# Performance work log

Measured on AMD Instinct MI355X. Metric: run time of the kernel, lower is better.

Reference implementation:

```python
import jax, jax.numpy as jnp
import numpy as np

B, T, DIM = 4, 1024, 512
H, DH, NK, K = 8, 128, 256, 16
LN_EPS = 1e-5


def setup_inputs() -> dict:
    key = jax.random.key(0)
    ks = jax.random.split(key, 5)
    std_q = 1.0 / np.sqrt(DIM)
    std_k = 1.0 / np.sqrt(DH)
    std_v = 1.0 / np.sqrt(DIM)
    x = jax.random.normal(ks[0], (B, T, DIM), dtype=jnp.float32)
    Wq = jax.random.normal(ks[1], (2 * H * DH, DIM), dtype=jnp.float32) * std_q
    ln_g = jnp.ones((DH,), dtype=jnp.float32)
    ln_b = jnp.zeros((DH,), dtype=jnp.float32)
    keys = jax.random.normal(ks[2], (H, NK, 2, DH), dtype=jnp.float32) * std_k
    values = jax.random.normal(ks[3], (NK * NK, DIM), dtype=jnp.float32) * std_v
    return {"x": x, "Wq": Wq, "ln_g": ln_g, "ln_b": ln_b, "keys": keys, "values": values}


def _layernorm(q, g, b):
    mu = q.mean(-1, keepdims=True)
    var = ((q - mu) ** 2).mean(-1, keepdims=True)
    return (q - mu) * jax.lax.rsqrt(var + LN_EPS) * g + b


def reference(x, Wq, ln_g, ln_b, keys, values):
    b, t, _ = x.shape
    # queries: [b, t, 2*h*dh] -> [b, t, p=2, h, dh]
    q = jnp.einsum('btd,qd->btq', x, Wq).reshape(b, t, 2, H, DH)
    q = _layernorm(q, ln_g, ln_b)
    # product-key dots: [b, t, h, p, n]
    dots = jnp.einsum('btphd,hnpd->bthpn', q, keys)
    scores, idx = jax.lax.top_k(dots, K)          # [b,t,h,2,K]
    sx, sy = scores[..., 0, :], scores[..., 1, :]
    ix, iy = idx[..., 0, :], idx[..., 1, :]
    # cross product of the two halves -> K*K candidates
    all_scores = (sx[..., :, None] + sy[..., None, :]).reshape(b, t, H, K * K)
    all_idx = (ix[..., :, None] * NK + iy[..., None, :]).reshape(b, t, H, K * K)
    final_scores, final_pos = jax.lax.top_k(all_scores, K)      # [b,t,h,K]
    value_idx = jnp.take_along_axis(all_idx, final_pos, axis=-1)
    attn = jax.nn.softmax(final_scores, axis=-1)
    value_idx = value_idx.reshape(b * t, H * K)
    attn = attn.reshape(b * t, H * K)
    # EmbeddingBag(sum) with per-sample weights
    gathered = values[value_idx]                  # [(b t), h*K, dim]
    out = jnp.einsum('nk,nkd->nd', attn, gathered)
    return out.reshape(b, t, DIM)
```

## Files before the change

### kernel.cpp

```cpp
#include <hip/hip_runtime.h>
#include <hip/hip_bf16.h>
#include <math.h>
#include <stdint.h>

#define BT   4096
#define QD   2048
#define DIMK 512
#define NH   8
#define DHD  128
#define NKEY 256
#define TK   16

__global__ __launch_bounds__(256) void qproj_ln(
    const float* __restrict__ x, const float* __restrict__ Wq,
    const float* __restrict__ lng, const float* __restrict__ lnb,
    float* __restrict__ q) {
  __shared__ float As[8][128];
  __shared__ float Bs[8][128];
  const int br = blockIdx.x;
  const int bc = blockIdx.y;
  const int tid = threadIdx.x;
  const int ty = tid >> 4, tx = tid & 15;
  const int lr = tid >> 1, lc = (tid & 1) * 4;

  const float* xA = x  + (size_t)(br * 128 + lr) * DIMK + lc;
  const float* wB = Wq + (size_t)(bc * 128 + lr) * DIMK + lc;

  float acc[8][8];
  #pragma unroll
  for (int i = 0; i < 8; i++)
    #pragma unroll
    for (int j = 0; j < 8; j++) acc[i][j] = 0.f;

  for (int kt = 0; kt < DIMK; kt += 8) {
    float4 a4 = *(const float4*)(xA + kt);
    float4 b4 = *(const float4*)(wB + kt);
    __syncthreads();
    As[lc + 0][lr] = a4.x; As[lc + 1][lr] = a4.y;
    As[lc + 2][lr] = a4.z; As[lc + 3][lr] = a4.w;
    Bs[lc + 0][lr] = b4.x; Bs[lc + 1][lr] = b4.y;
    Bs[lc + 2][lr] = b4.z; Bs[lc + 3][lr] = b4.w;
    __syncthreads();
    #pragma unroll
    for (int kk = 0; kk < 8; kk++) {
      float a[8], b[8];
      #pragma unroll
      for (int i = 0; i < 8; i++) a[i] = As[kk][ty * 8 + i];
      #pragma unroll
      for (int j = 0; j < 8; j++) b[j] = Bs[kk][tx * 8 + j];
      #pragma unroll
      for (int i = 0; i < 8; i++)
        #pragma unroll
        for (int j = 0; j < 8; j++)
          acc[i][j] = fmaf(a[i], b[j], acc[i][j]);
    }
  }

  float g[8], bb[8];
  #pragma unroll
  for (int j = 0; j < 8; j++) { g[j] = lng[tx * 8 + j]; bb[j] = lnb[tx * 8 + j]; }

  #pragma unroll
  for (int i = 0; i < 8; i++) {
    float s = 0.f;
    #pragma unroll
    for (int j = 0; j < 8; j++) s += acc[i][j];
    #pragma unroll
    for (int m = 1; m < 16; m <<= 1) s += __shfl_xor(s, m);
    const float mu = s * (1.f / 128.f);
    float s2 = 0.f;
    #pragma unroll
    for (int j = 0; j < 8; j++) { float d = acc[i][j] - mu; s2 = fmaf(d, d, s2); }
    #pragma unroll
    for (int m = 1; m < 16; m <<= 1) s2 += __shfl_xor(s2, m);
    const float rstd = rsqrtf(s2 * (1.f / 128.f) + 1e-5f);
    float o[8];
    #pragma unroll
    for (int j = 0; j < 8; j++)
      o[j] = (acc[i][j] - mu) * rstd * g[j] + bb[j];
    float* qp = q + (size_t)(br * 128 + ty * 8 + i) * QD + bc * 128 + tx * 8;
    *(float4*)(qp)     = make_float4(o[0], o[1], o[2], o[3]);
    *(float4*)(qp + 4) = make_float4(o[4], o[5], o[6], o[7]);
  }
}

__global__ __launch_bounds__(256) void dots_gemm(
    const float* __restrict__ q, const float* __restrict__ keys,
    float* __restrict__ S) {
  __shared__ float As[8][128];
  __shared__ float Bs[8][128];
  const int br = blockIdx.x;
  const int bc = blockIdx.y;
  const int hp = blockIdx.z;
  const int h = hp >> 1, p = hp & 1;
  const int tid = threadIdx.x;
  const int ty = tid >> 4, tx = tid & 15;
  const int lr = tid >> 1, lc = (tid & 1) * 4;

  const float* qA = q + (size_t)(br * 128 + lr) * QD + p * 1024 + h * 128 + lc;
  const float* kB = keys + ((size_t)((h * 256 + bc * 128 + lr) * 2 + p)) * 128 + lc;

  float acc[8][8];
  #pragma unroll
  for (int i = 0; i < 8; i++)
    #pragma unroll
    for (int j = 0; j < 8; j++) acc[i][j] = 0.f;

  for (int kt = 0; kt < DHD; kt += 8) {
    float4 a4 = *(const float4*)(qA + kt);
    float4 b4 = *(const float4*)(kB + kt);
    __syncthreads();
    As[lc + 0][lr] = a4.x; As[lc + 1][lr] = a4.y;
    As[lc + 2][lr] = a4.z; As[lc + 3][lr] = a4.w;
    Bs[lc + 0][lr] = b4.x; Bs[lc + 1][lr] = b4.y;
    Bs[lc + 2][lr] = b4.z; Bs[lc + 3][lr] = b4.w;
    __syncthreads();
    #pragma unroll
    for (int kk = 0; kk < 8; kk++) {
      float a[8], b[8];
      #pragma unroll
      for (int i = 0; i < 8; i++) a[i] = As[kk][ty * 8 + i];
      #pragma unroll
      for (int j = 0; j < 8; j++) b[j] = Bs[kk][tx * 8 + j];
      #pragma unroll
      for (int i = 0; i < 8; i++)
        #pragma unroll
        for (int j = 0; j < 8; j++)
          acc[i][j] = fmaf(a[i], b[j], acc[i][j]);
    }
  }

  float* Sp = S + (size_t)hp * BT * NKEY;
  #pragma unroll
  for (int i = 0; i < 8; i++) {
    float* pp = Sp + (size_t)(br * 128 + ty * 8 + i) * NKEY + bc * 128 + tx * 8;
    *(float4*)(pp)     = make_float4(acc[i][0], acc[i][1], acc[i][2], acc[i][3]);
    *(float4*)(pp + 4) = make_float4(acc[i][4], acc[i][5], acc[i][6], acc[i][7]);
  }
}

__device__ __forceinline__ uint32_t f2u(float f) {
  uint32_t b = __float_as_uint(f);
  return b ^ ((uint32_t)((int32_t)b >> 31) | 0x80000000u);
}
__device__ __forceinline__ float u2f(uint32_t u) {
  uint32_t b = (u & 0x80000000u) ? (u ^ 0x80000000u) : ~u;
  return __uint_as_float(b);
}
__device__ __forceinline__ int cnt_lt(uint64_t m) {
  return __builtin_amdgcn_mbcnt_hi((uint32_t)(m >> 32),
         __builtin_amdgcn_mbcnt_lo((uint32_t)m, 0));
}

__global__ __launch_bounds__(64) void topk_combine(
    const float* __restrict__ S, float* __restrict__ W, int* __restrict__ I) {
  const int bt = blockIdx.x;
  const int h  = blockIdx.y;
  const int l  = threadIdx.x;

  __shared__ __align__(16) float sx_lds[16], sy_lds[16], w_lds[16];
  __shared__ __align__(16) int   ix_lds[16], iy_lds[16], vi_lds[16];

  const float* S0 = S + ((size_t)(h * 2 + 0) * BT + bt) * NKEY;
  const float* S1 = S + ((size_t)(h * 2 + 1) * BT + bt) * NKEY;
  float4 v0 = *(const float4*)(S0 + l * 4);
  float4 v1 = *(const float4*)(S1 + l * 4);
  float s0[4] = {v0.x, v0.y, v0.z, v0.w};
  float s1[4] = {v1.x, v1.y, v1.z, v1.w};
  uint32_t u0[4], u1[4];
  #pragma unroll
  for (int r = 0; r < 4; r++) { u0[r] = f2u(s0[r]); u1[r] = f2u(s1[r]); }

  uint32_t pfx0 = 0u, pfx1 = 0u;
  #pragma unroll
  for (int b = 31; b >= 0; b--) {
    const uint32_t t0 = pfx0 | (1u << b);
    const uint32_t t1 = pfx1 | (1u << b);
    int c0 = 0, c1 = 0;
    #pragma unroll
    for (int r = 0; r < 4; r++) {
      c0 += __popcll(__ballot(u0[r] >= t0));
      c1 += __popcll(__ballot(u1[r] >= t1));
    }
    if (c0 >= TK) pfx0 = t0;
    if (c1 >= TK) pfx1 = t1;
  }

  {
    uint64_t mgt[4], meq[4];
    int ngt = 0, below_gt = 0, below_eq = 0;
    #pragma unroll
    for (int r = 0; r < 4; r++) {
      mgt[r] = __ballot(u0[r] > pfx0);
      meq[r] = __ballot(u0[r] == pfx0);
      ngt += __popcll(mgt[r]);
      below_gt += cnt_lt(mgt[r]);
      below_eq += cnt_lt(meq[r]);
    }
    const int need = TK - ngt;
    int loc_gt = 0, loc_eq = 0;
    #pragma unroll
    for (int r = 0; r < 4; r++) {
      const bool isgt = (u0[r] > pfx0), iseq = (u0[r] == pfx0);
      int slot = -1;
      if (isgt) slot = below_gt + loc_gt;
      else if (iseq) { const int re = below_eq + loc_eq; if (re < need) slot = ngt + re; }
      if (slot >= 0) { sx_lds[slot] = s0[r]; ix_lds[slot] = l * 4 + r; }
      loc_gt += isgt; loc_eq += iseq;
    }
  }
  {
    uint64_t mgt[4], meq[4];
    int ngt = 0, below_gt = 0, below_eq = 0;
    #pragma unroll
    for (int r = 0; r < 4; r++) {
      mgt[r] = __ballot(u1[r] > pfx1);
      meq[r] = __ballot(u1[r] == pfx1);
      ngt += __popcll(mgt[r]);
      below_gt += cnt_lt(mgt[r]);
      below_eq += cnt_lt(meq[r]);
    }
    const int need = TK - ngt;
    int loc_gt = 0, loc_eq = 0;
    #pragma unroll
    for (int r = 0; r < 4; r++) {
      const bool isgt = (u1[r] > pfx1), iseq = (u1[r] == pfx1);
      int slot = -1;
      if (isgt) slot = below_gt + loc_gt;
      else if (iseq) { const int re = below_eq + loc_eq; if (re < need) slot = ngt + re; }
      if (slot >= 0) { sy_lds[slot] = s1[r]; iy_lds[slot] = l * 4 + r; }
      loc_gt += isgt; loc_eq += iseq;
    }
  }
  __syncthreads();

  const float sxv = sx_lds[l >> 2];
  const float4 syv = *(const float4*)&sy_lds[(l & 3) * 4];
  float cv[4] = {sxv + syv.x, sxv + syv.y, sxv + syv.z, sxv + syv.w};
  uint32_t uc[4];
  #pragma unroll
  for (int r = 0; r < 4; r++) uc[r] = f2u(cv[r]);

  uint32_t pfx2 = 0u;
  #pragma unroll
  for (int b = 31; b >= 0; b--) {
    const uint32_t t2 = pfx2 | (1u << b);
    int c2 = 0;
    #pragma unroll
    for (int r = 0; r < 4; r++) c2 += __popcll(__ballot(uc[r] >= t2));
    if (c2 >= TK) pfx2 = t2;
  }

  const float tau2f = u2f(pfx2);
  const int ivx = ix_lds[l >> 2];
  const int4 iyv = *(const int4*)&iy_lds[(l & 3) * 4];
  const int iy4[4] = {iyv.x, iyv.y, iyv.z, iyv.w};
  {
    uint64_t mgt[4], meq[4];
    int ngt = 0, below_gt = 0, below_eq = 0;
    #pragma unroll
    for (int r = 0; r < 4; r++) {
      mgt[r] = __ballot(uc[r] > pfx2);
      meq[r] = __ballot(uc[r] == pfx2);
      ngt += __popcll(mgt[r]);
      below_gt += cnt_lt(mgt[r]);
      below_eq += cnt_lt(meq[r]);
    }
    const int need = TK - ngt;
    int loc_gt = 0, loc_eq = 0;
    #pragma unroll
    for (int r = 0; r < 4; r++) {
      const bool isgt = (uc[r] > pfx2), iseq = (uc[r] == pfx2);
      int slot = -1;
      if (isgt) slot = below_gt + loc_gt;
      else if (iseq) { const int re = below_eq + loc_eq; if (re < need) slot = ngt + re; }
      if (slot >= 0) {
        w_lds[slot]  = __expf(cv[r] - tau2f);
        vi_lds[slot] = ivx * NKEY + iy4[r];
      }
      loc_gt += isgt; loc_eq += iseq;
    }
  }
  __syncthreads();

  if (l < TK) {
    const float4 wa = *(const float4*)&w_lds[0];
    const float4 wb = *(const float4*)&w_lds[4];
    const float4 wc = *(const float4*)&w_lds[8];
    const float4 wd = *(const float4*)&w_lds[12];
    const float sum = (wa.x + wa.y + wa.z + wa.w) + (wb.x + wb.y + wb.z + wb.w)
                    + (wc.x + wc.y + wc.z + wc.w) + (wd.x + wd.y + wd.z + wd.w);
    const size_t o = ((size_t)bt * NH + h) * TK + l;
    W[o] = w_lds[l] / sum;
    I[o] = vi_lds[l];
  }
}

__global__ __launch_bounds__(128) void gather_out(
    const float* __restrict__ values, const float* __restrict__ W,
    const int* __restrict__ I, float* __restrict__ out) {
  const int bt = blockIdx.x;
  const int t  = threadIdx.x;
  __shared__ float wsm[128];
  __shared__ int   ism[128];
  wsm[t] = W[(size_t)bt * 128 + t];
  ism[t] = I[(size_t)bt * 128 + t];
  __syncthreads();
  float4 acc = make_float4(0.f, 0.f, 0.f, 0.f);
  #pragma unroll 4
  for (int r = 0; r < 128; r++) {
    const float w = wsm[r];
    const float4 v = *(const float4*)(values + (size_t)ism[r] * DIMK + t * 4);
    acc.x = fmaf(w, v.x, acc.x);
    acc.y = fmaf(w, v.y, acc.y);
    acc.z = fmaf(w, v.z, acc.z);
    acc.w = fmaf(w, v.w, acc.w);
  }
  *(float4*)(out + (size_t)bt * DIMK + t * 4) = acc;
}

extern "C" void kernel_launch(void* const* d_in, const int* in_sizes, int n_in,
                              void* d_out, int out_size, void* d_ws, size_t ws_size,
                              hipStream_t stream) {
  const float* x      = (const float*)d_in[0];
  const float* Wq     = (const float*)d_in[1];
  const float* lng    = (const float*)d_in[2];
  const float* lnb    = (const float*)d_in[3];
  const float* keys   = (const float*)d_in[4];
  const float* values = (const float*)d_in[5];
  float* out = (float*)d_out;

  char* ws = (char*)d_ws;
  float* q = (float*)(ws);
  float* S = (float*)(ws + (size_t)32 * 1024 * 1024);
  float* W = (float*)(ws + (size_t)96 * 1024 * 1024);
  int*   I = (int*)  (ws + (size_t)98 * 1024 * 1024);

  qproj_ln    <<<dim3(32, 16),    256, 0, stream>>>(x, Wq, lng, lnb, q);
  dots_gemm   <<<dim3(32, 2, 16), 256, 0, stream>>>(q, keys, S);
  topk_combine<<<dim3(4096, 8),   64,  0, stream>>>(S, W, I);
  gather_out  <<<dim3(4096),      128, 0, stream>>>(values, W, I, out);
}
```

Measured before the change: 549.6 us.

## Double-buffer shared memory in both FP32 GEMMs with deeper K tiles

Both the Q-projection and the key-dots GEMMs now use two shared-memory buffers with a 16-wide K tile. The next tile's global loads are issued before computing on the current one, which removes one barrier per iteration and overlaps load latency with FMAs. The B-operand column mapping changes from 8 contiguous columns per thread to two groups of 4 at offsets tx*4 and 64+tx*4, to reduce LDS bank conflicts and keep output stores coalesced. Shared memory per block grows fourfold, which may reduce occupancy.

```diff
diff --git a/kernel.cpp b/kernel.cpp
--- a/kernel.cpp
+++ b/kernel.cpp
@@ -11,17 +11,18 @@
 #define NKEY 256
 #define TK   16
 
+
 __global__ __launch_bounds__(256) void qproj_ln(
     const float* __restrict__ x, const float* __restrict__ Wq,
     const float* __restrict__ lng, const float* __restrict__ lnb,
     float* __restrict__ q) {
-  __shared__ float As[8][128];
-  __shared__ float Bs[8][128];
+  __shared__ float As[2][16][128];
+  __shared__ float Bs[2][16][128];
   const int br = blockIdx.x;
   const int bc = blockIdx.y;
   const int tid = threadIdx.x;
   const int ty = tid >> 4, tx = tid & 15;
-  const int lr = tid >> 1, lc = (tid & 1) * 4;
+  const int lr = tid >> 1, lc = (tid & 1) * 8;
 
   const float* xA = x  + (size_t)(br * 128 + lr) * DIMK + lc;
   const float* wB = Wq + (size_t)(bc * 128 + lr) * DIMK + lc;
@@ -32,33 +33,59 @@
     #pragma unroll
     for (int j = 0; j < 8; j++) acc[i][j] = 0.f;
 
-  for (int kt = 0; kt < DIMK; kt += 8) {
-    float4 a4 = *(const float4*)(xA + kt);
-    float4 b4 = *(const float4*)(wB + kt);
-    __syncthreads();
-    As[lc + 0][lr] = a4.x; As[lc + 1][lr] = a4.y;
-    As[lc + 2][lr] = a4.z; As[lc + 3][lr] = a4.w;
-    Bs[lc + 0][lr] = b4.x; Bs[lc + 1][lr] = b4.y;
-    Bs[lc + 2][lr] = b4.z; Bs[lc + 3][lr] = b4.w;
-    __syncthreads();
-    #pragma unroll
-    for (int kk = 0; kk < 8; kk++) {
+  float4 pa0 = *(const float4*)(xA);
+  float4 pa1 = *(const float4*)(xA + 4);
+  float4 pb0 = *(const float4*)(wB);
+  float4 pb1 = *(const float4*)(wB + 4);
+  {
+    const float va[8] = {pa0.x,pa0.y,pa0.z,pa0.w,pa1.x,pa1.y,pa1.z,pa1.w};
+    const float vb[8] = {pb0.x,pb0.y,pb0.z,pb0.w,pb1.x,pb1.y,pb1.z,pb1.w};
+    #pragma unroll
+    for (int i = 0; i < 8; i++) { As[0][lc + i][lr] = va[i]; Bs[0][lc + i][lr] = vb[i]; }
+  }
+  __syncthreads();
+
+  for (int kt = 0; kt < 32; kt++) {
+    const int cur = kt & 1;
+    const bool more = (kt + 1) < 32;
+    if (more) {
+      const int ko = (kt + 1) * 16;
+      pa0 = *(const float4*)(xA + ko);
+      pa1 = *(const float4*)(xA + ko + 4);
+      pb0 = *(const float4*)(wB + ko);
+      pb1 = *(const float4*)(wB + ko + 4);
+    }
+    #pragma unroll
+    for (int kk = 0; kk < 16; kk++) {
       float a[8], b[8];
       #pragma unroll
-      for (int i = 0; i < 8; i++) a[i] = As[kk][ty * 8 + i];
-      #pragma unroll
-      for (int j = 0; j < 8; j++) b[j] = Bs[kk][tx * 8 + j];
+      for (int i = 0; i < 8; i++) a[i] = As[cur][kk][ty * 8 + i];
+      #pragma unroll
+      for (int j = 0; j < 4; j++) {
+        b[j]     = Bs[cur][kk][tx * 4 + j];
+        b[4 + j] = Bs[cur][kk][64 + tx * 4 + j];
+      }
       #pragma unroll
       for (int i = 0; i < 8; i++)
         #pragma unroll
         for (int j = 0; j < 8; j++)
           acc[i][j] = fmaf(a[i], b[j], acc[i][j]);
     }
+    if (more) {
+      const float va[8] = {pa0.x,pa0.y,pa0.z,pa0.w,pa1.x,pa1.y,pa1.z,pa1.w};
+      const float vb[8] = {pb0.x,pb0.y,pb0.z,pb0.w,pb1.x,pb1.y,pb1.z,pb1.w};
+      #pragma unroll
+      for (int i = 0; i < 8; i++) { As[cur ^ 1][lc + i][lr] = va[i]; Bs[cur ^ 1][lc + i][lr] = vb[i]; }
+      __syncthreads();
+    }
   }
 
   float g[8], bb[8];
   #pragma unroll
-  for (int j = 0; j < 8; j++) { g[j] = lng[tx * 8 + j]; bb[j] = lnb[tx * 8 + j]; }
+  for (int j = 0; j < 4; j++) {
+    g[j]      = lng[tx * 4 + j];      bb[j]     = lnb[tx * 4 + j];
+    g[4 + j]  = lng[64 + tx * 4 + j]; bb[4 + j] = lnb[64 + tx * 4 + j];
+  }
 
   #pragma unroll
   for (int i = 0; i < 8; i++) {
@@ -70,7 +97,7 @@
     const float mu = s * (1.f / 128.f);
     float s2 = 0.f;
     #pragma unroll
-    for (int j = 0; j < 8; j++) { float d = acc[i][j] - mu; s2 = fmaf(d, d, s2); }
+    for (int j = 0; j < 8; j++) { const float d = acc[i][j] - mu; s2 = fmaf(d, d, s2); }
     #pragma unroll
     for (int m = 1; m < 16; m <<= 1) s2 += __shfl_xor(s2, m);
     const float rstd = rsqrtf(s2 * (1.f / 128.f) + 1e-5f);
@@ -78,24 +105,24 @@
     #pragma unroll
     for (int j = 0; j < 8; j++)
       o[j] = (acc[i][j] - mu) * rstd * g[j] + bb[j];
-    float* qp = q + (size_t)(br * 128 + ty * 8 + i) * QD + bc * 128 + tx * 8;
-    *(float4*)(qp)     = make_float4(o[0], o[1], o[2], o[3]);
-    *(float4*)(qp + 4) = make_float4(o[4], o[5], o[6], o[7]);
+    float* qp = q + (size_t)(br * 128 + ty * 8 + i) * QD + bc * 128;
+    *(float4*)(qp + tx * 4)      = make_float4(o[0], o[1], o[2], o[3]);
+    *(float4*)(qp + 64 + tx * 4) = make_float4(o[4], o[5], o[6], o[7]);
   }
 }
 
 __global__ __launch_bounds__(256) void dots_gemm(
     const float* __restrict__ q, const float* __restrict__ keys,
     float* __restrict__ S) {
-  __shared__ float As[8][128];
-  __shared__ float Bs[8][128];
+  __shared__ float As[2][16][128];
+  __shared__ float Bs[2][16][128];
   const int br = blockIdx.x;
   const int bc = blockIdx.y;
   const int hp = blockIdx.z;
   const int h = hp >> 1, p = hp & 1;
   const int tid = threadIdx.x;
   const int ty = tid >> 4, tx = tid & 15;
-  const int lr = tid >> 1, lc = (tid & 1) * 4;
+  const int lr = tid >> 1, lc = (tid & 1) * 8;
 
   const float* qA = q + (size_t)(br * 128 + lr) * QD + p * 1024 + h * 128 + lc;
   const float* kB = keys + ((size_t)((h * 256 + bc * 128 + lr) * 2 + p)) * 128 + lc;
@@ -106,36 +133,59 @@
     #pragma unroll
     for (int j = 0; j < 8; j++) acc[i][j] = 0.f;
 
-  for (int kt = 0; kt < DHD; kt += 8) {
-    float4 a4 = *(const float4*)(qA + kt);
-    float4 b4 = *(const float4*)(kB + kt);
-    __syncthreads();
-    As[lc + 0][lr] = a4.x; As[lc + 1][lr] = a4.y;
-    As[lc + 2][lr] = a4.z; As[lc + 3][lr] = a4.w;
-    Bs[lc + 0][lr] = b4.x; Bs[lc + 1][lr] = b4.y;
-    Bs[lc + 2][lr] = b4.z; Bs[lc + 3][lr] = b4.w;
-    __syncthreads();
-    #pragma unroll
-    for (int kk = 0; kk < 8; kk++) {
+  float4 pa0 = *(const float4*)(qA);
+  float4 pa1 = *(const float4*)(qA + 4);
+  float4 pb0 = *(const float4*)(kB);
+  float4 pb1 = *(const float4*)(kB + 4);
+  {
+    const float va[8] = {pa0.x,pa0.y,pa0.z,pa0.w,pa1.x,pa1.y,pa1.z,pa1.w};
+    const float vb[8] = {pb0.x,pb0.y,pb0.z,pb0.w,pb1.x,pb1.y,pb1.z,pb1.w};
+    #pragma unroll
+    for (int i = 0; i < 8; i++) { As[0][lc + i][lr] = va[i]; Bs[0][lc + i][lr] = vb[i]; }
+  }
+  __syncthreads();
+
+  for (int kt = 0; kt < 8; kt++) {
+    const int cur = kt & 1;
+    const bool more = (kt + 1) < 8;
+    if (more) {
+      const int ko = (kt + 1) * 16;
+      pa0 = *(const float4*)(qA + ko);
+      pa1 = *(const float4*)(qA + ko + 4);
+      pb0 = *(const float4*)(kB + ko);
+      pb1 = *(const float4*)(kB + ko + 4);
+    }
+    #pragma unroll
+    for (int kk = 0; kk < 16; kk++) {
       float a[8], b[8];
       #pragma unroll
-      for (int i = 0; i < 8; i++) a[i] = As[kk][ty * 8 + i];
-      #pragma unroll
-      for (int j = 0; j < 8; j++) b[j] = Bs[kk][tx * 8 + j];
+      for (int i = 0; i < 8; i++) a[i] = As[cur][kk][ty * 8 + i];
+      #pragma unroll
+      for (int j = 0; j < 4; j++) {
+        b[j]     = Bs[cur][kk][tx * 4 + j];
+        b[4 + j] = Bs[cur][kk][64 + tx * 4 + j];
+      }
       #pragma unroll
       for (int i = 0; i < 8; i++)
         #pragma unroll
         for (int j = 0; j < 8; j++)
           acc[i][j] = fmaf(a[i], b[j], acc[i][j]);
     }
+    if (more) {
+      const float va[8] = {pa0.x,pa0.y,pa0.z,pa0.w,pa1.x,pa1.y,pa1.z,pa1.w};
+      const float vb[8] = {pb0.x,pb0.y,pb0.z,pb0.w,pb1.x,pb1.y,pb1.z,pb1.w};
+      #pragma unroll
+      for (int i = 0; i < 8; i++) { As[cur ^ 1][lc + i][lr] = va[i]; Bs[cur ^ 1][lc + i][lr] = vb[i]; }
+      __syncthreads();
+    }
   }
 
   float* Sp = S + (size_t)hp * BT * NKEY;
   #pragma unroll
   for (int i = 0; i < 8; i++) {
-    float* pp = Sp + (size_t)(br * 128 + ty * 8 + i) * NKEY + bc * 128 + tx * 8;
-    *(float4*)(pp)     = make_float4(acc[i][0], acc[i][1], acc[i][2], acc[i][3]);
-    *(float4*)(pp + 4) = make_float4(acc[i][4], acc[i][5], acc[i][6], acc[i][7]);
+    float* pp = Sp + (size_t)(br * 128 + ty * 8 + i) * NKEY + bc * 128;
+    *(float4*)(pp + tx * 4)      = make_float4(acc[i][0], acc[i][1], acc[i][2], acc[i][3]);
+    *(float4*)(pp + 64 + tx * 4) = make_float4(acc[i][4], acc[i][5], acc[i][6], acc[i][7]);
   }
 }
 
@@ -331,10 +381,11 @@
   float* out = (float*)d_out;
 
   char* ws = (char*)d_ws;
+  const size_t MB = 1024 * 1024;
   float* q = (float*)(ws);
-  float* S = (float*)(ws + (size_t)32 * 1024 * 1024);
-  float* W = (float*)(ws + (size_t)96 * 1024 * 1024);
-  int*   I = (int*)  (ws + (size_t)98 * 1024 * 1024);
+  float* S = (float*)(ws + 32 * MB);
+  float* W = (float*)(ws + 96 * MB);
+  int*   I = (int*)  (ws + 98 * MB);
 
   qproj_ln    <<<dim3(32, 16),    256, 0, stream>>>(x, Wq, lng, lnb, q);
   dots_gemm   <<<dim3(32, 2, 16), 256, 0, stream>>>(q, keys, S);
```

Measured after the change: 608.4 us. 1.11x slower.
